# Optimization experiments

Measured on AMD Instinct MI355X. Metric: run time of the kernel, lower is better.

## Reference

```python
import jax, jax.numpy as jnp
import numpy as np

NH = 2  # attention heads


def _mha(q, k, v, w, b, pool):
    """2-head attention; w:[4,D,D] (q,k,v,o as x@W), b:[4,D], pool:[Lq] pools query axis -> [B,D]."""
    B, Lq, D = q.shape
    dk = D // NH
    Q = (q @ w[0] + b[0]).reshape(B, Lq, NH, dk).transpose(0, 2, 1, 3)
    K = (k @ w[1] + b[1]).reshape(B, -1, NH, dk).transpose(0, 2, 1, 3)
    V = (v @ w[2] + b[2]).reshape(B, -1, NH, dk).transpose(0, 2, 1, 3)
    scores = jnp.einsum('bhqd,bhkd->bhqk', Q, K) / jnp.sqrt(jnp.asarray(dk, q.dtype))
    attn = jax.nn.softmax(scores, axis=-1)
    ctx = jnp.einsum('bhqk,bhkd->bqhd', attn, V).reshape(B, Lq, D)
    out = ctx @ w[3] + b[3]              # [B, Lq, D]
    return jnp.einsum('bqd,q->bd', out, pool)  # pooled over query axis (w_size)


def setup_inputs() -> dict:
    key = jax.random.key(0)
    ks = jax.random.split(key, 32)
    B, T, D, N = 64, 32, 768, 901
    s = 0.02
    inp = {
        'question_embeds': jax.random.normal(ks[0], (B, T, D), jnp.float32),
        'image_local_embeds': jax.random.normal(ks[1], (B, N, D), jnp.float32),
        'h0': jax.random.uniform(ks[2], (B, D), jnp.float32),
        'gru_w_ih': jax.random.normal(ks[3], (3 * D, D), jnp.float32) * s,
        'gru_w_hh': jax.random.normal(ks[4], (3 * D, D), jnp.float32) * s,
        'gru_b_ih': jax.random.normal(ks[5], (3 * D,), jnp.float32) * s,
        'gru_b_hh': jax.random.normal(ks[6], (3 * D,), jnp.float32) * s,
        'ga_w': jax.random.normal(ks[7], (4, D, D), jnp.float32) * s,
        'ga_b': jax.random.normal(ks[8], (4, D), jnp.float32) * s,
        'ga_pool': jax.random.normal(ks[9], (1,), jnp.float32),
        'la_w': jax.random.normal(ks[10], (4, D, D), jnp.float32) * s,
        'la_b': jax.random.normal(ks[11], (4, D), jnp.float32) * s,
        'la_pool': jax.random.normal(ks[12], (T,), jnp.float32) * 0.2,
        'go_w': jax.random.normal(ks[13], (4, D, D), jnp.float32) * s,
        'go_b': jax.random.normal(ks[14], (4, D), jnp.float32) * s,
        'go_pool': jax.random.normal(ks[15], (T,), jnp.float32) * 0.2,
        'f1_w': jax.random.normal(ks[16], (2 * D, 1024), jnp.float32) * s,
        'f1_b': jax.random.normal(ks[17], (1024,), jnp.float32) * s,
        'f2_w': jax.random.normal(ks[18], (1024, 512), jnp.float32) * s,
        'f2_b': jax.random.normal(ks[19], (512,), jnp.float32) * s,
        'f3_w': jax.random.normal(ks[20], (512, 1024), jnp.float32) * s,
        'f3_b': jax.random.normal(ks[21], (1024,), jnp.float32) * s,
    }
    return inp


def reference(question_embeds, image_local_embeds, h0,
              gru_w_ih, gru_w_hh, gru_b_ih, gru_b_hh,
              ga_w, ga_b, ga_pool, la_w, la_b, la_pool,
              go_w, go_b, go_pool,
              f1_w, f1_b, f2_w, f2_b, f3_w, f3_b):
    img_cls = image_local_embeds[:, :1, :]        # [B,1,D] global CLS token
    img_loc = image_local_embeds[:, 1:, :]        # [B,N-1,D] patch tokens
    Hs = h0.shape[-1]

    def step(h, x_t):
        # per-timestep cross-attention of question token against image CLS
        a = _mha(x_t[:, None, :], img_cls, img_cls, ga_w, ga_b, ga_pool)  # [B,D]
        wx = a @ gru_w_ih.T                      # [B,3H]
        wh = h @ gru_w_hh.T
        r = jax.nn.sigmoid(wx[:, :Hs] + wh[:, :Hs] + gru_b_ih[:Hs] + gru_b_hh[:Hs])
        z = jax.nn.sigmoid(wx[:, Hs:2 * Hs] + wh[:, Hs:2 * Hs]
                           + gru_b_ih[Hs:2 * Hs] + gru_b_hh[Hs:2 * Hs])
        n = jnp.tanh(wx[:, 2 * Hs:] + gru_b_ih[2 * Hs:]
                     + r * (wh[:, 2 * Hs:] + gru_b_hh[2 * Hs:]))
        h_new = (1 - z) * n + z * h
        return h_new, h_new

    xs = jnp.swapaxes(question_embeds, 0, 1)      # [T,B,D]
    _, ys = jax.lax.scan(step, h0, xs)
    q_emb = jnp.swapaxes(ys, 0, 1)                # [B,T,D]

    local_out = _mha(q_emb, img_loc, img_loc, la_w, la_b, la_pool)   # [B,D]
    gobal_out = _mha(q_emb, img_cls, img_cls, go_w, go_b, go_pool)   # [B,D]
    h = jnp.concatenate([local_out, gobal_out], axis=1)              # [B,2D]
    x = h @ f1_w + f1_b
    x = jax.nn.relu(x @ f2_w + f2_b)
    return x @ f3_w + f3_b                                           # [B,1024]
```

## Files before the change

### kernel.cpp

```cpp
#include <hip/hip_runtime.h>
#include <math.h>


typedef short bf16x8 __attribute__((ext_vector_type(8)));
typedef float f32x4 __attribute__((ext_vector_type(4)));
typedef unsigned short ushort_t;

#define GRU_NB 48

__device__ __forceinline__ unsigned short f2b(float f) {
    unsigned int u = __float_as_uint(f);
    unsigned int r = (u + 0x7FFFu + ((u >> 16) & 1u)) >> 16;
    return (unsigned short)r;
}
__device__ __forceinline__ float b2f(unsigned short s) {
    return __uint_as_float(((unsigned int)s) << 16);
}
__device__ __forceinline__ float sigm(float x) { return 1.f / (1.f + __expf(-x)); }
__device__ __forceinline__ float tanhx(float x) {
    x = fminf(fmaxf(x, -15.f), 15.f);
    float e = __expf(2.f * x);
    return (e - 1.f) / (e + 1.f);
}

__device__ __forceinline__ void gbar(int* flags, int nb, int phase, int bid, int tid) {
    __syncthreads();
    if (tid == 0) __hip_atomic_store(&flags[bid], phase, __ATOMIC_RELAXED, __HIP_MEMORY_SCOPE_AGENT);
    if (tid < 64) {
        for (;;) {
            int v = 0x7fffffff;
            for (int f = tid; f < nb; f += 64)
                v = min(v, __hip_atomic_load(&flags[f], __ATOMIC_RELAXED, __HIP_MEMORY_SCOPE_AGENT));
            if (__all(v >= phase)) break;
            __builtin_amdgcn_s_sleep(1);
        }
    }
    __syncthreads();
}


__global__ void k_cvt_all(const float* __restrict__ whh, const float* __restrict__ la0,
                          const float* __restrict__ la1, const float* __restrict__ h0,
                          const float* __restrict__ gp, const float* __restrict__ lp,
                          ushort_t* __restrict__ whhb, ushort_t* __restrict__ law0b,
                          ushort_t* __restrict__ law1b, ushort_t* __restrict__ h0b,
                          float* __restrict__ hbuf, float* __restrict__ scal,
                          int* __restrict__ bar) {
    if (blockIdx.x == 0) {
        int t = threadIdx.x;
        if (t < 64) {
            float v1 = (t < 32) ? gp[t] : 0.f;
            float v2 = (t < 32) ? lp[t] : 0.f;
#pragma unroll
            for (int m = 1; m < 32; m <<= 1) { v1 += __shfl_xor(v1, m, 64); v2 += __shfl_xor(v2, m, 64); }
            if (t == 0) { scal[0] = v1; scal[1] = v2; }
        }
        for (int i = threadIdx.x; i < 1024; i += 256) bar[i] = 0;
    }
    long i = (long)blockIdx.x * 256 + threadIdx.x;
    const long n1 = 2304L * 768, n2 = n1 + 768L * 768, n3 = n2 + 768L * 768, n4 = n3 + 64L * 768;
    if (i < n1) whhb[i] = f2b(whh[i]);
    else if (i < n2) law0b[i - n1] = f2b(la0[i - n1]);
    else if (i < n3) law1b[i - n2] = f2b(la1[i - n2]);
    else if (i < n4) { float v = h0[i - n3]; h0b[i - n3] = f2b(v); hbuf[i - n3] = v; }
}


template<int MR>
__device__ __forceinline__ void tgemm4(
    const float* __restrict__ A, long lda,
    const float* __restrict__ Bm, int ldb, int transB,
    const float* __restrict__ bias, float s1, float s2,
    const float* __restrict__ bias2, int b2lim,
    float* __restrict__ C, int ldc, int K, int relu, int agent,
    int m0, int n0, float* As, int tid)
{
    for (int r = 0; r < MR; r++)
        for (int k = tid; k < K; k += 256)
            As[r * K + k] = A[(long)(m0 + r) * lda + k];
    __syncthreads();
    int cl = tid & 63, kc = tid >> 6;
    int c = n0 + cl;
    int K4 = K >> 2;
    int kb = kc * K4;
    const float* Bp = transB ? (Bm + (long)c * ldb) : (Bm + c);
    float acc[MR];
#pragma unroll
    for (int r = 0; r < MR; r++) acc[r] = 0.f;
    for (int k = kb; k < kb + K4; k += 8) {
        float bv[8];
        if (!transB) {
#pragma unroll
            for (int i = 0; i < 8; i++) bv[i] = Bp[(long)(k + i) * ldb];
        } else {
            float4 q0 = *(const float4*)(Bp + k);
            float4 q1 = *(const float4*)(Bp + k + 4);
            bv[0] = q0.x; bv[1] = q0.y; bv[2] = q0.z; bv[3] = q0.w;
            bv[4] = q1.x; bv[5] = q1.y; bv[6] = q1.z; bv[7] = q1.w;
        }
#pragma unroll
        for (int i = 0; i < 8; i += 4) {
#pragma unroll
            for (int r = 0; r < MR; r++) {
                float4 x = *(const float4*)&As[r * K + k + i];
                acc[r] += x.x * bv[i] + x.y * bv[i + 1] + x.z * bv[i + 2] + x.w * bv[i + 3];
            }
        }
    }
    __syncthreads();
    float* Red = As;
#pragma unroll
    for (int r = 0; r < MR; r++) Red[(kc * MR + r) * 64 + cl] = acc[r];
    __syncthreads();
    {
        int rg = tid >> 6;
        float bb = (bias ? bias[c] * s2 : 0.f) + ((bias2 && c < b2lim) ? bias2[c] : 0.f);
#pragma unroll
        for (int i = 0; i < MR / 4; i++) {
            int r = rg + i * 4;
            float sum = (Red[(0 * MR + r) * 64 + cl] + Red[(1 * MR + r) * 64 + cl])
                      + (Red[(2 * MR + r) * 64 + cl] + Red[(3 * MR + r) * 64 + cl]);
            float o = sum * s1 + bb;
            if (relu) o = fmaxf(o, 0.f);
            if (agent) __hip_atomic_store(&C[(long)(m0 + r) * ldc + c], o,
                                          __ATOMIC_RELAXED, __HIP_MEMORY_SCOPE_AGENT);
            else C[(long)(m0 + r) * ldc + c] = o;
        }
    }
}


struct HeadP {
    const float *img, *ga_w2, *ga_b2, *go_w2, *go_b2;
    const float *ga_w3, *ga_b3, *go_w3, *go_b3;
    const float *ga_pool, *scal, *w_ih, *b_ih, *b_hh;
    float *t12, *t12g, *avec, *hcat, *base;
    int* flags; int p0, p1;
};

__global__ void __launch_bounds__(256) k_head(HeadP P) {
    __shared__ __align__(16) float As[16 * 768];
    int bid = blockIdx.x, tid = threadIdx.x;
    for (int p = P.p0; p <= P.p1; p++) {
        if (p == 1) {
            if (bid < 192) {
                int prob = bid / 96, r = bid % 96, m8 = r / 12, ct = r % 12;
                tgemm4<8>(P.img, 901L * 768, prob ? P.go_w2 : P.ga_w2, 768, 0,
                          prob ? P.go_b2 : P.ga_b2, 1.f, 1.f, nullptr, 0,
                          prob ? P.t12g : P.t12, 768, 768, 0, 1, m8 * 8, ct * 64, As, tid);
            }
        } else if (p == 2) {
            if (bid < 192) {
                int prob = bid / 96, r = bid % 96, m8 = r / 12, ct = r % 12;
                float sc = prob ? P.scal[0] : P.ga_pool[0];
                tgemm4<8>(prob ? P.t12g : P.t12, 768, prob ? P.go_w3 : P.ga_w3, 768, 0,
                          prob ? P.go_b3 : P.ga_b3, sc, sc, nullptr, 0,
                          prob ? (P.hcat + 768) : P.avec, prob ? 1536 : 768, 768, 0, 1,
                          m8 * 8, ct * 64, As, tid);
            }
        } else if (p == 3) {
            if (bid < 144) {
                int m4 = bid / 36, ct = bid % 36;
                tgemm4<16>(P.avec, 768, P.w_ih, 768, 1, P.b_ih, 1.f, 1.f, P.b_hh, 1536,
                           P.base, 2304, 768, 0, 0, m4 * 16, ct * 64, As, tid);
            }
        }
        if (p < P.p1) gbar(P.flags, 192, p, bid, tid);
    }
}


struct GruP {
    const ushort_t* h0b; const float* h0f; const ushort_t* whh;
    const float* base; const float* bhh; ushort_t* qemb; int* flags;
};

__global__ void __launch_bounds__(384) k_gru_coop(GruP P) {
    __shared__ __align__(16) ushort_t whh_s[3][16][776];
    __shared__ __align__(16) ushort_t as_s[64][200];
    __shared__ float bs[3][64][20];
    __shared__ float h_s[64][20];
    __shared__ float bhh_s[16];
    float* gs = (float*)&as_s[0][0];
    int tid = threadIdx.x;
    int wid = tid >> 6, lane = tid & 63, quad = lane >> 4, l16 = lane & 15;
    int g = wid >> 1, mh = wid & 1;
    int j = blockIdx.x, d0 = j * 16;
    {
        int gS = (wid < 3) ? wid : wid - 3;
        int r0 = (wid < 3) ? 0 : 8;
        for (int r = r0; r < r0 + 8; r++)
            for (int kk = lane * 8; kk < 768; kk += 512)
                *(bf16x8*)&whh_s[gS][r][kk] = *(const bf16x8*)&P.whh[(size_t)(gS * 768 + d0 + r) * 768 + kk];
    }
    for (int e = tid; e < 3072; e += 384) {
        int g2 = e >> 10, rem = e & 1023, b = rem >> 4, c = rem & 15;
        bs[g2][b][c] = P.base[b * 2304 + g2 * 768 + d0 + c];
    }
    for (int e = tid; e < 1024; e += 384) {
        int b = e >> 4, c = e & 15;
        h_s[b][c] = P.h0f[b * 768 + d0 + c];
    }
    if (tid < 16) bhh_s[tid] = P.bhh[1536 + d0 + tid];
    __syncthreads();
    for (int t = 0; t < 32; t++) {
        const ushort_t* Ap = (t == 0) ? P.h0b : (P.qemb + (size_t)(t - 1) * 768);
        size_t ldA = (t == 0) ? 768 : (size_t)32 * 768;
        f32x4 zz4 = {0.f, 0.f, 0.f, 0.f};
        f32x4 acc[2];
        acc[0] = zz4; acc[1] = zz4;
        for (int kq = 0; kq < 4; kq++) {
            __syncthreads();
#pragma unroll
            for (int i = 0; i < 4; i++) {
                int id = i * 384 + tid;
                int row = id / 24, c = id % 24;
                *(bf16x8*)&as_s[row][c * 8] =
                    *(const bf16x8*)(Ap + (size_t)row * ldA + kq * 192 + c * 8);
            }
            __syncthreads();
            for (int kk = 0; kk < 192; kk += 32) {
                bf16x8 bfr = *(const bf16x8*)&whh_s[g][l16][kq * 192 + kk + quad * 8];
#pragma unroll
                for (int mi = 0; mi < 2; mi++) {
                    bf16x8 af = *(const bf16x8*)&as_s[mh * 32 + mi * 16 + l16][kk + quad * 8];
                    acc[mi] = __builtin_amdgcn_mfma_f32_16x16x32_bf16(af, bfr, acc[mi], 0, 0, 0);
                }
            }
        }
        __syncthreads();
#pragma unroll
        for (int mi = 0; mi < 2; mi++)
#pragma unroll
            for (int r = 0; r < 4; r++)
                gs[((size_t)g * 64 + mh * 32 + mi * 16 + quad * 4 + r) * 20 + l16] = acc[mi][r];
        __syncthreads();
        for (int e = tid; e < 512; e += 384) {
            int b = e >> 3, c0 = (e & 7) * 2;
            float hn[2];
#pragma unroll
            for (int u = 0; u < 2; u++) {
                int c = c0 + u;
                float g0 = gs[((size_t)0 * 64 + b) * 20 + c];
                float g1 = gs[((size_t)1 * 64 + b) * 20 + c];
                float g2v = gs[((size_t)2 * 64 + b) * 20 + c];
                float rr = sigm(g0 + bs[0][b][c]);
                float zg = sigm(g1 + bs[1][b][c]);
                float nn = tanhx(bs[2][b][c] + rr * (g2v + bhh_s[c]));
                float hv = h_s[b][c];
                hn[u] = (1.f - zg) * nn + zg * hv;
                h_s[b][c] = hn[u];
            }
            unsigned int pk = (unsigned int)f2b(hn[0]) | ((unsigned int)f2b(hn[1]) << 16);
            __hip_atomic_store((unsigned int*)&P.qemb[((size_t)b * 32 + t) * 768 + d0 + c0],
                               pk, __ATOMIC_RELAXED, __HIP_MEMORY_SCOPE_AGENT);
        }
        __syncthreads();
        if (t < 31) {
            if (tid == 0)
                __hip_atomic_store(&P.flags[j], t + 1, __ATOMIC_RELAXED, __HIP_MEMORY_SCOPE_AGENT);
            if (tid < 64) {
                for (;;) {
                    int v = (tid < GRU_NB)
                        ? __hip_atomic_load(&P.flags[tid], __ATOMIC_RELAXED, __HIP_MEMORY_SCOPE_AGENT)
                        : 0x7fffffff;
                    if (__all(v > t)) break;
                    __builtin_amdgcn_s_sleep(1);
                }
            }
            __syncthreads();
        }
    }
}

__global__ void __launch_bounds__(256) k_gru_step(
    int t, const ushort_t* h0b, const ushort_t* whh, const float* base,
    const float* bhh, float* h, ushort_t* qemb)
{
    int wv = threadIdx.x >> 6, lane = threadIdx.x & 63;
    int quad = lane >> 4, l16 = lane & 15;
    int d0 = blockIdx.x * 64 + wv * 16;
    float bhhn = bhh[1536 + d0 + l16];
    const ushort_t* Ap = (t == 0) ? h0b : (qemb + (long)(t - 1) * 768);
    long ldA = (t == 0) ? 768 : 32 * 768;
    int d = d0 + l16;
    f32x4 zz4 = {0.f, 0.f, 0.f, 0.f};
    f32x4 acc[3][4];
#pragma unroll
    for (int g = 0; g < 3; g++)
#pragma unroll
        for (int mi = 0; mi < 4; mi++) acc[g][mi] = zz4;
    for (int kk = 0; kk < 768; kk += 32) {
        bf16x8 af[4];
#pragma unroll
        for (int mi = 0; mi < 4; mi++)
            af[mi] = *(const bf16x8*)(Ap + (long)(mi * 16 + l16) * ldA + kk + quad * 8);
#pragma unroll
        for (int g = 0; g < 3; g++) {
            bf16x8 bfr = *(const bf16x8*)(whh + (long)(g * 768 + d0 + l16) * 768 + kk + quad * 8);
#pragma unroll
            for (int mi = 0; mi < 4; mi++)
                acc[g][mi] = __builtin_amdgcn_mfma_f32_16x16x32_bf16(af[mi], bfr, acc[g][mi], 0, 0, 0);
        }
    }
#pragma unroll
    for (int mi = 0; mi < 4; mi++) {
#pragma unroll
        for (int r = 0; r < 4; r++) {
            int b = mi * 16 + quad * 4 + r;
            const float* bb = base + b * 2304;
            float rr = sigm(acc[0][mi][r] + bb[d]);
            float zg = sigm(acc[1][mi][r] + bb[768 + d]);
            float nn = tanhx(bb[1536 + d] + rr * (acc[2][mi][r] + bhhn));
            float hv = h[b * 768 + d];
            float hnew = (1.f - zg) * nn + zg * hv;
            h[b * 768 + d] = hnew;
            qemb[(long)(b * 32 + t) * 768 + d] = f2b(hnew);
        }
    }
}


__global__ void __launch_bounds__(256) k_gemm_bf16(
    const ushort_t* __restrict__ A, int lda,
    const ushort_t* __restrict__ B, int ldb, int transB,
    const float* __restrict__ bias,
    ushort_t* __restrict__ Cb, int ldc,
    int K, int remap, int rowoff)
{
    __shared__ __align__(16) ushort_t As[64][72];
    __shared__ __align__(16) ushort_t Bs[64][72];
    int tid = threadIdx.x;
    int wv = tid >> 6, lane = tid & 63, quad = lane >> 4, l16 = lane & 15;
    long bm = (long)blockIdx.y * 64, bn = (long)blockIdx.x * 64;
    f32x4 zz4 = {0.f, 0.f, 0.f, 0.f};
    f32x4 acc[4];
#pragma unroll
    for (int mi = 0; mi < 4; mi++) acc[mi] = zz4;
    int row4 = tid >> 2, seg = tid & 3;
    for (int k0 = 0; k0 < K; k0 += 64) {
        {
            const ushort_t* src = A + (bm + row4) * lda + k0 + seg * 16;
            *(bf16x8*)&As[row4][seg * 16] = *(const bf16x8*)src;
            *(bf16x8*)&As[row4][seg * 16 + 8] = *(const bf16x8*)(src + 8);
        }
        if (transB) {
            const ushort_t* src = B + (bn + row4) * ldb + k0 + seg * 16;
            *(bf16x8*)&Bs[row4][seg * 16] = *(const bf16x8*)src;
            *(bf16x8*)&Bs[row4][seg * 16 + 8] = *(const bf16x8*)(src + 8);
        } else {
            const ushort_t* src = B + (long)(k0 + row4) * ldb + bn + seg * 16;
            bf16x8 v0 = *(const bf16x8*)src;
            bf16x8 v1 = *(const bf16x8*)(src + 8);
#pragma unroll
            for (int i = 0; i < 8; i++) {
                Bs[seg * 16 + i][row4] = (ushort_t)v0[i];
                Bs[seg * 16 + 8 + i][row4] = (ushort_t)v1[i];
            }
        }
        __syncthreads();
#pragma unroll
        for (int ks = 0; ks < 64; ks += 32) {
            bf16x8 bfr = *(const bf16x8*)&Bs[wv * 16 + l16][ks + quad * 8];
#pragma unroll
            for (int mi = 0; mi < 4; mi++) {
                bf16x8 af = *(const bf16x8*)&As[mi * 16 + l16][ks + quad * 8];
                acc[mi] = __builtin_amdgcn_mfma_f32_16x16x32_bf16(af, bfr, acc[mi], 0, 0, 0);
            }
        }
        __syncthreads();
    }
    int ncol = (int)bn + wv * 16 + l16;
    float bv = bias ? bias[ncol] : 0.f;
#pragma unroll
    for (int mi = 0; mi < 4; mi++) {
#pragma unroll
        for (int r = 0; r < 4; r++) {
            long row = bm + mi * 16 + quad * 4 + r;
            long orow = remap ? ((row >> 5) * 64 + rowoff + (row & 31)) : row;
            Cb[orow * ldc + ncol] = f2b(acc[mi][r] + bv);
        }
    }
}


__global__ void __launch_bounds__(512) k_flash(
    const float* __restrict__ img, const ushort_t* __restrict__ Qt,
    const ushort_t* __restrict__ Qb, const float* __restrict__ la_b1,
    float* __restrict__ pm, float* __restrict__ pl,
    ushort_t* __restrict__ pacc, int nsplit)
{
    __shared__ __align__(16) ushort_t xs[32][776];
    __shared__ float Sls[64][36];
    __shared__ __align__(16) ushort_t Pls[64][40];
    __shared__ float m_s[64], l_s[64], al_s[64], qb_s[64];
    int b = blockIdx.x;
    int sp = blockIdx.y;
    int tper = (29 + nsplit - 1) / nsplit;
    int tb = sp * tper, te = min(29, tb + tper);
    int tid = threadIdx.x;
    int wv = tid >> 6, lane = tid & 63, quad = lane >> 4, l16 = lane & 15;
    {
        int row = tid >> 3, sub = tid & 7;
        int hh = row >> 5, q = row & 31;
        const ushort_t* src = Qb + ((size_t)(b * 32 + q)) * 768 + hh * 384 + sub * 48;
        const float* bb = la_b1 + hh * 384 + sub * 48;
        float s = 0.f;
#pragma unroll
        for (int k = 0; k < 48; k++) s += b2f(src[k]) * bb[k];
        s += __shfl_xor(s, 1, 64); s += __shfl_xor(s, 2, 64); s += __shfl_xor(s, 4, 64);
        if (sub == 0) qb_s[row] = s;
    }
    if (tid < 64) { m_s[tid] = -1e30f; l_s[tid] = 0.f; }
    f32x4 zz4 = {0.f, 0.f, 0.f, 0.f};
    f32x4 acc[4][6];
#pragma unroll
    for (int mi = 0; mi < 4; mi++)
#pragma unroll
        for (int nj = 0; nj < 6; nj++) acc[mi][nj] = zz4;
    const float rs = 0.051031036307982884f;
    int smi = wv & 3, sni = wv >> 2;
    __syncthreads();
    for (int t0 = tb; t0 < te; t0++) {
        int key0 = t0 * 32;
        {
            int keyl = tid >> 4, dseg = tid & 15;
            int key = key0 + keyl;
            const float* src = img + ((long)b * 901 + 1 + key) * 768;
            bool ok = key < 900;
#pragma unroll
            for (int c = 0; c < 12; c++) {
                int dd = c * 64 + dseg * 4;
                float x0 = 0, x1 = 0, x2 = 0, x3 = 0;
                if (ok) { float4 v = *(const float4*)(src + dd); x0 = v.x; x1 = v.y; x2 = v.z; x3 = v.w; }
                ushort_t* dst = &xs[keyl][dd];
                dst[0] = f2b(x0); dst[1] = f2b(x1); dst[2] = f2b(x2); dst[3] = f2b(x3);
            }
        }
        __syncthreads();
        {
            f32x4 as = zz4;
            const ushort_t* qrow = Qt + (long)(b * 64 + smi * 16 + l16) * 768 + quad * 8;
            const ushort_t* xrow = &xs[sni * 16 + l16][quad * 8];
#pragma unroll
            for (int kk = 0; kk < 768; kk += 32) {
                bf16x8 aq = *(const bf16x8*)(qrow + kk);
                bf16x8 bx = *(const bf16x8*)(xrow + kk);
                as = __builtin_amdgcn_mfma_f32_16x16x32_bf16(aq, bx, as, 0, 0, 0);
            }
#pragma unroll
            for (int r = 0; r < 4; r++) {
                int row = smi * 16 + quad * 4 + r;
                Sls[row][sni * 16 + l16] = (as[r] + qb_s[row]) * rs;
            }
        }
        __syncthreads();
        {
            int row = tid >> 3, sub = tid & 7;
            float sv[4];
            float mx = -1e30f;
#pragma unroll
            for (int i = 0; i < 4; i++) {
                int kl = sub + i * 8;
                float s = (key0 + kl < 900) ? Sls[row][kl] : -1e30f;
                sv[i] = s; mx = fmaxf(mx, s);
            }
            mx = fmaxf(mx, __shfl_xor(mx, 1, 64));
            mx = fmaxf(mx, __shfl_xor(mx, 2, 64));
            mx = fmaxf(mx, __shfl_xor(mx, 4, 64));
            float mold = m_s[row];
            float mnew = fmaxf(mold, mx);
            float ss = 0.f;
#pragma unroll
            for (int i = 0; i < 4; i++) {
                float p = __expf(sv[i] - mnew);
                ss += p;
                Pls[row][sub + i * 8] = f2b(p);
            }
            ss += __shfl_xor(ss, 1, 64);
            ss += __shfl_xor(ss, 2, 64);
            ss += __shfl_xor(ss, 4, 64);
            if (sub == 0) {
                float alpha = __expf(mold - mnew);
                al_s[row] = alpha;
                l_s[row] = l_s[row] * alpha + ss;
                m_s[row] = mnew;
            }
        }
        __syncthreads();
        {
            bf16x8 pf[4];
#pragma unroll
            for (int mi = 0; mi < 4; mi++)
                pf[mi] = *(const bf16x8*)&Pls[mi * 16 + l16][quad * 8];
#pragma unroll
            for (int mi = 0; mi < 4; mi++) {
#pragma unroll
                for (int r = 0; r < 4; r++) {
                    float a = al_s[mi * 16 + quad * 4 + r];
#pragma unroll
                    for (int nj = 0; nj < 6; nj++) acc[mi][nj][r] *= a;
                }
            }
#pragma unroll
            for (int nj = 0; nj < 6; nj++) {
                int dd = wv * 96 + nj * 16 + l16;
                bf16x8 bx;
#pragma unroll
                for (int j = 0; j < 8; j++) bx[j] = (short)xs[quad * 8 + j][dd];
#pragma unroll
                for (int mi = 0; mi < 4; mi++)
                    acc[mi][nj] = __builtin_amdgcn_mfma_f32_16x16x32_bf16(pf[mi], bx, acc[mi][nj], 0, 0, 0);
            }
        }
        __syncthreads();
    }
    if (tid < 64) {
        pm[(b * nsplit + sp) * 64 + tid] = m_s[tid];
        pl[(b * nsplit + sp) * 64 + tid] = l_s[tid];
    }
#pragma unroll
    for (int mi = 0; mi < 4; mi++) {
#pragma unroll
        for (int r = 0; r < 4; r++) {
            int row = mi * 16 + quad * 4 + r;
            ushort_t* dst = pacc + ((size_t)(b * nsplit + sp) * 64 + row) * 768;
#pragma unroll
            for (int nj = 0; nj < 6; nj++)
                dst[wv * 96 + nj * 16 + l16] = f2b(acc[mi][nj][r]);
        }
    }
}


struct TailP {
    const float *pm, *pl; const ushort_t* pacc; const float* lp;
    const float *la_w2, *la_b2, *la_w3, *la_b3, *scal;
    float *plX, *pc, *hcat;
    const float *f1w, *f1b, *f2w, *f2b, *f3w, *f3b;
    float *x1, *x2, *out;
    int* flags; int p0, p1, nsplit;
};

template<int NS>
__global__ void __launch_bounds__(256) k_tail(TailP P) {
    __shared__ __align__(16) float As[4 * 1536];
    __shared__ float cw[NS][64];
    int bid = blockIdx.x, tid = threadIdx.x;
    float sla = P.scal[1];
    for (int p = P.p0; p <= P.p1; p++) {
        if (p == 0) {
            if (bid < 192) {
                int b = bid / 3, jj = bid % 3;
                if (tid < 64) {
                    int row = tid;
                    float ex[NS];
                    float mmax = -1e30f;
#pragma unroll
                    for (int s = 0; s < NS; s++) mmax = fmaxf(mmax, P.pm[(b * NS + s) * 64 + row]);
                    float lsum = 0.f;
#pragma unroll
                    for (int s = 0; s < NS; s++) {
                        ex[s] = __expf(P.pm[(b * NS + s) * 64 + row] - mmax);
                        lsum += ex[s] * P.pl[(b * NS + s) * 64 + row];
                    }
                    float sc = P.lp[row & 31] / lsum;
#pragma unroll
                    for (int s = 0; s < NS; s++) cw[s][row] = ex[s] * sc;
                }
                __syncthreads();
                int col = jj * 256 + tid;
                const ushort_t* pp = P.pacc + ((size_t)(b * NS)) * 64 * 768 + col;
                float ac0 = 0.f, ac1 = 0.f;
                for (int q = 0; q < 32; q += 2) {
                    float vv[2][NS][2];
#pragma unroll
                    for (int u = 0; u < 2; u++)
#pragma unroll
                        for (int s = 0; s < NS; s++) {
                            vv[u][s][0] = b2f(pp[((size_t)(s * 64 + q + u)) * 768]);
                            vv[u][s][1] = b2f(pp[((size_t)(s * 64 + 32 + q + u)) * 768]);
                        }
#pragma unroll
                    for (int u = 0; u < 2; u++)
#pragma unroll
                        for (int s = 0; s < NS; s++) {
                            ac0 += cw[s][q + u] * vv[u][s][0];
                            ac1 += cw[s][32 + q + u] * vv[u][s][1];
                        }
                }
                __hip_atomic_store(&P.plX[b * 1536 + col], ac0,
                                   __ATOMIC_RELAXED, __HIP_MEMORY_SCOPE_AGENT);
                __hip_atomic_store(&P.plX[b * 1536 + 768 + col], ac1,
                                   __ATOMIC_RELAXED, __HIP_MEMORY_SCOPE_AGENT);
            }
        } else if (p == 1) {
            if (bid < 192) {
                int m4 = bid / 12, ct = bid % 12, prob = ct / 6;
                tgemm4<4>(P.plX + prob * 768, 1536, P.la_w2, 768, 0,
                          P.la_b2, 1.f, sla, nullptr, 0,
                          P.pc, 768, 768, 0, 1, m4 * 4, ct * 64, As, tid);
            }
        } else if (p == 2) {
            if (bid < 192) {
                int m4 = bid / 12, ct = bid % 12;
                tgemm4<4>(P.pc, 768, P.la_w3, 768, 0, P.la_b3, 1.f, sla, nullptr, 0,
                          P.hcat, 1536, 768, 0, 1, m4 * 4, ct * 64, As, tid);
            }
        } else if (p == 3) {
            if (bid < 256) {
                int m4 = bid / 16, ct = bid % 16;
                tgemm4<4>(P.hcat, 1536, P.f1w, 1024, 0, P.f1b, 1.f, 1.f, nullptr, 0,
                          P.x1, 1024, 1536, 0, 1, m4 * 4, ct * 64, As, tid);
            }
        } else if (p == 4) {
            if (bid < 128) {
                int m4 = bid / 8, ct = bid % 8;
                tgemm4<4>(P.x1, 1024, P.f2w, 512, 0, P.f2b, 1.f, 1.f, nullptr, 0,
                          P.x2, 512, 1024, 1, 1, m4 * 4, ct * 64, As, tid);
            }
        } else if (p == 5) {
            if (bid < 256) {
                int m4 = bid / 16, ct = bid % 16;
                tgemm4<4>(P.x2, 512, P.f3w, 1024, 0, P.f3b, 1.f, 1.f, nullptr, 0,
                          P.out, 1024, 512, 0, 0, m4 * 4, ct * 64, As, tid);
            }
        }
        if (p < P.p1) gbar(P.flags, 256, p + 1, bid, tid);
    }
}


extern "C" void kernel_launch(void* const* d_in, const int* in_sizes, int n_in,
                              void* d_out, int out_size, void* d_ws, size_t ws_size,
                              hipStream_t stream)
{
    const float* img  = (const float*)d_in[1];
    const float* h0   = (const float*)d_in[2];
    const float* w_ih = (const float*)d_in[3];
    const float* w_hh = (const float*)d_in[4];
    const float* b_ih = (const float*)d_in[5];
    const float* b_hh = (const float*)d_in[6];
    const float* ga_w = (const float*)d_in[7];
    const float* ga_b = (const float*)d_in[8];
    const float* ga_pool = (const float*)d_in[9];
    const float* la_w = (const float*)d_in[10];
    const float* la_b = (const float*)d_in[11];
    const float* la_pool = (const float*)d_in[12];
    const float* go_w = (const float*)d_in[13];
    const float* go_b = (const float*)d_in[14];
    const float* go_pool = (const float*)d_in[15];
    const float* f1w = (const float*)d_in[16];
    const float* f1b = (const float*)d_in[17];
    const float* f2w = (const float*)d_in[18];
    const float* f2b_ = (const float*)d_in[19];
    const float* f3w = (const float*)d_in[20];
    const float* f3b = (const float*)d_in[21];
    float* out = (float*)d_out;
    (void)in_sizes; (void)n_in; (void)out_size;

    int nsplit = (ws_size >= (size_t)43 * 1024 * 1024) ? 4 : 2;

    char* w = (char*)d_ws;
    auto alloc = [&](size_t bytes) -> char* {
        char* p = w; w += (bytes + 255) & ~(size_t)255; return p;
    };
    float*    scal  = (float*)alloc(256);
    int*      bar   = (int*)alloc(4096);
    ushort_t* law0b = (ushort_t*)alloc((size_t)768 * 768 * 2);
    ushort_t* law1b = (ushort_t*)alloc((size_t)768 * 768 * 2);
    ushort_t* h0b   = (ushort_t*)alloc((size_t)64 * 768 * 2);
    ushort_t* qembb = (ushort_t*)alloc((size_t)2048 * 768 * 2);
    ushort_t* Qb    = (ushort_t*)alloc((size_t)2048 * 768 * 2);
    ushort_t* Qtb   = (ushort_t*)alloc((size_t)4096 * 768 * 2);
    float*    pm    = (float*)alloc((size_t)64 * 4 * 64 * 4);
    float*    pl    = (float*)alloc((size_t)64 * 4 * 64 * 4);
    float*    plX   = (float*)alloc((size_t)64 * 1536 * 4);
    float*    pc    = (float*)alloc((size_t)64 * 768 * 4);
    float*    hcat  = (float*)alloc((size_t)64 * 1536 * 4);
    float*    x1    = (float*)alloc((size_t)64 * 1024 * 4);
    float*    x2    = (float*)alloc((size_t)64 * 512 * 4);
    char* uni = w;
    char* u = uni;
    auto ualloc = [&](size_t bytes) -> char* {
        char* p = u; u += (bytes + 255) & ~(size_t)255; return p;
    };
    ushort_t* whhb  = (ushort_t*)ualloc((size_t)2304 * 768 * 2);
    float*    t12   = (float*)ualloc((size_t)2 * 64 * 768 * 4);
    float*    avec  = (float*)ualloc((size_t)64 * 768 * 4);
    float*    base  = (float*)ualloc((size_t)64 * 2304 * 4);
    float*    hbuf  = (float*)ualloc((size_t)64 * 768 * 4);
    ushort_t* pacc  = (ushort_t*)uni;
    float*    t12g  = t12 + 64 * 768;

    const float* ga_w2 = ga_w + 2 * 768 * 768; const float* ga_w3 = ga_w + 3 * 768 * 768;
    const float* ga_b2 = ga_b + 2 * 768;       const float* ga_b3 = ga_b + 3 * 768;
    const float* go_w2 = go_w + 2 * 768 * 768; const float* go_w3 = go_w + 3 * 768 * 768;
    const float* go_b2 = go_b + 2 * 768;       const float* go_b3 = go_b + 3 * 768;
    const float* la_w0 = la_w;                 const float* la_w1 = la_w + 768 * 768;
    const float* la_w2 = la_w + 2 * 768 * 768; const float* la_w3 = la_w + 3 * 768 * 768;
    const float* la_b0 = la_b;                 const float* la_b1 = la_b + 768;
    const float* la_b2 = la_b + 2 * 768;       const float* la_b3 = la_b + 3 * 768;

    dim3 blk(256);
    k_cvt_all<<<11712, blk, 0, stream>>>(w_hh, la_w0, la_w1, h0, go_pool, la_pool,
                                         whhb, law0b, law1b, h0b, hbuf, scal, bar);

    {
        HeadP P;
        P.img = img; P.ga_w2 = ga_w2; P.ga_b2 = ga_b2; P.go_w2 = go_w2; P.go_b2 = go_b2;
        P.ga_w3 = ga_w3; P.ga_b3 = ga_b3; P.go_w3 = go_w3; P.go_b3 = go_b3;
        P.ga_pool = ga_pool; P.scal = scal; P.w_ih = w_ih; P.b_ih = b_ih; P.b_hh = b_hh;
        P.t12 = t12; P.t12g = t12g; P.avec = avec; P.hcat = hcat; P.base = base;
        P.flags = bar + 64; P.p0 = 1; P.p1 = 3;
        void* args[1] = { &P };
        hipError_t e = hipLaunchCooperativeKernel((void*)k_head, dim3(192), blk, args, 0, stream);
        if (e != hipSuccess)
            for (int p = 1; p <= 3; p++) { P.p0 = P.p1 = p; k_head<<<192, blk, 0, stream>>>(P); }
    }

    {
        GruP P;
        P.h0b = h0b; P.h0f = h0; P.whh = whhb; P.base = base; P.bhh = b_hh;
        P.qemb = qembb; P.flags = bar;
        void* args[1] = { &P };
        hipError_t e = hipLaunchCooperativeKernel((void*)k_gru_coop, dim3(GRU_NB), dim3(384),
                                                  args, 0, stream);
        if (e != hipSuccess)
            for (int t = 0; t < 32; t++)
                k_gru_step<<<12, blk, 0, stream>>>(t, h0b, whhb, base, b_hh, hbuf, qembb);
    }

    k_gemm_bf16<<<dim3(12, 32), blk, 0, stream>>>(qembb, 768, law0b, 768, 0, la_b0, Qb, 768, 768, 0, 0);
    k_gemm_bf16<<<dim3(12, 32), blk, 0, stream>>>(Qb, 768, law1b, 768, 1, nullptr, Qtb, 768, 384, 1, 0);
    k_gemm_bf16<<<dim3(12, 32), blk, 0, stream>>>(Qb + 384, 768, law1b + 384, 768, 1, nullptr, Qtb, 768, 384, 1, 32);

    k_flash<<<dim3(64, nsplit), dim3(512), 0, stream>>>(img, Qtb, Qb, la_b1, pm, pl, pacc, nsplit);

    {
        TailP P;
        P.pm = pm; P.pl = pl; P.pacc = pacc; P.lp = la_pool;
        P.la_w2 = la_w2; P.la_b2 = la_b2; P.la_w3 = la_w3; P.la_b3 = la_b3; P.scal = scal;
        P.plX = plX; P.pc = pc; P.hcat = hcat;
        P.f1w = f1w; P.f1b = f1b; P.f2w = f2w; P.f2b = f2b_; P.f3w = f3w; P.f3b = f3b;
        P.x1 = x1; P.x2 = x2; P.out = out;
        P.flags = bar + 320; P.p0 = 0; P.p1 = 5; P.nsplit = nsplit;
        void* args[1] = { &P };
        if (nsplit == 4) {
            hipError_t e = hipLaunchCooperativeKernel((void*)k_tail<4>, dim3(256), blk, args, 0, stream);
            if (e != hipSuccess)
                for (int p = 0; p <= 5; p++) { P.p0 = P.p1 = p; k_tail<4><<<256, blk, 0, stream>>>(P); }
        } else {
            hipError_t e = hipLaunchCooperativeKernel((void*)k_tail<2>, dim3(256), blk, args, 0, stream);
            if (e != hipSuccess)
                for (int p = 0; p <= 5; p++) { P.p0 = P.p1 = p; k_tail<2><<<256, blk, 0, stream>>>(P); }
        }
    }
}
```

Before: 1.006 ms.

## Double tail kernel grid to 512 blocks with 2-row GEMM tiles

```diff
diff --git a/kernel.cpp b/kernel.cpp
--- a/kernel.cpp
+++ b/kernel.cpp
@@ -112,20 +112,16 @@
 #pragma unroll
     for (int r = 0; r < MR; r++) Red[(kc * MR + r) * 64 + cl] = acc[r];
     __syncthreads();
-    {
-        int rg = tid >> 6;
-        float bb = (bias ? bias[c] * s2 : 0.f) + ((bias2 && c < b2lim) ? bias2[c] : 0.f);
-#pragma unroll
-        for (int i = 0; i < MR / 4; i++) {
-            int r = rg + i * 4;
-            float sum = (Red[(0 * MR + r) * 64 + cl] + Red[(1 * MR + r) * 64 + cl])
-                      + (Red[(2 * MR + r) * 64 + cl] + Red[(3 * MR + r) * 64 + cl]);
-            float o = sum * s1 + bb;
-            if (relu) o = fmaxf(o, 0.f);
-            if (agent) __hip_atomic_store(&C[(long)(m0 + r) * ldc + c], o,
-                                          __ATOMIC_RELAXED, __HIP_MEMORY_SCOPE_AGENT);
-            else C[(long)(m0 + r) * ldc + c] = o;
-        }
+    for (int o = tid; o < MR * 64; o += 256) {
+        int r = o >> 6, c2 = o & 63, cc = n0 + c2;
+        float sum = (Red[(0 * MR + r) * 64 + c2] + Red[(1 * MR + r) * 64 + c2])
+                  + (Red[(2 * MR + r) * 64 + c2] + Red[(3 * MR + r) * 64 + c2]);
+        float bb = (bias ? bias[cc] * s2 : 0.f) + ((bias2 && cc < b2lim) ? bias2[cc] : 0.f);
+        float ov = sum * s1 + bb;
+        if (relu) ov = fmaxf(ov, 0.f);
+        if (agent) __hip_atomic_store(&C[(long)(m0 + r) * ldc + cc], ov,
+                                      __ATOMIC_RELAXED, __HIP_MEMORY_SCOPE_AGENT);
+        else C[(long)(m0 + r) * ldc + cc] = ov;
     }
 }
 
@@ -543,17 +539,17 @@
 };
 
 template<int NS>
-__global__ void __launch_bounds__(256) k_tail(TailP P) {
-    __shared__ __align__(16) float As[4 * 1536];
-    __shared__ float cw[NS][64];
+__global__ void __launch_bounds__(256, 4) k_tail(TailP P) {
+    __shared__ __align__(16) float As[2 * 1536];
+    __shared__ float cw[NS][32];
     int bid = blockIdx.x, tid = threadIdx.x;
     float sla = P.scal[1];
     for (int p = P.p0; p <= P.p1; p++) {
         if (p == 0) {
-            if (bid < 192) {
-                int b = bid / 3, jj = bid % 3;
-                if (tid < 64) {
-                    int row = tid;
+            if (bid < 384) {
+                int b = bid / 6, r6 = bid % 6, jj = r6 % 3, half = r6 / 3;
+                if (tid < 32) {
+                    int row = half * 32 + tid;
                     float ex[NS];
                     float mmax = -1e30f;
 #pragma unroll
@@ -564,69 +560,65 @@
                         ex[s] = __expf(P.pm[(b * NS + s) * 64 + row] - mmax);
                         lsum += ex[s] * P.pl[(b * NS + s) * 64 + row];
                     }
-                    float sc = P.lp[row & 31] / lsum;
-#pragma unroll
-                    for (int s = 0; s < NS; s++) cw[s][row] = ex[s] * sc;
+                    float sc = P.lp[tid] / lsum;
+#pragma unroll
+                    for (int s = 0; s < NS; s++) cw[s][tid] = ex[s] * sc;
                 }
                 __syncthreads();
                 int col = jj * 256 + tid;
-                const ushort_t* pp = P.pacc + ((size_t)(b * NS)) * 64 * 768 + col;
-                float ac0 = 0.f, ac1 = 0.f;
+                const ushort_t* pp = P.pacc + ((size_t)(b * NS)) * 64 * 768
+                                   + (size_t)half * 32 * 768 + col;
+                float ac = 0.f;
                 for (int q = 0; q < 32; q += 2) {
-                    float vv[2][NS][2];
+                    float vv[2][NS];
 #pragma unroll
                     for (int u = 0; u < 2; u++)
 #pragma unroll
-                        for (int s = 0; s < NS; s++) {
-                            vv[u][s][0] = b2f(pp[((size_t)(s * 64 + q + u)) * 768]);
-                            vv[u][s][1] = b2f(pp[((size_t)(s * 64 + 32 + q + u)) * 768]);
-                        }
+                        for (int s = 0; s < NS; s++)
+                            vv[u][s] = b2f(pp[((size_t)(s * 64 + q + u)) * 768]);
 #pragma unroll
                     for (int u = 0; u < 2; u++)
 #pragma unroll
-                        for (int s = 0; s < NS; s++) {
-                            ac0 += cw[s][q + u] * vv[u][s][0];
-                            ac1 += cw[s][32 + q + u] * vv[u][s][1];
-                        }
+                        for (int s = 0; s < NS; s++)
+                            ac += cw[s][q + u] * vv[u][s];
                 }
-                __hip_atomic_store(&P.plX[b * 1536 + col], ac0,
+                __hip_atomic_store(&P.plX[b * 1536 + half * 768 + col], ac,
                                    __ATOMIC_RELAXED, __HIP_MEMORY_SCOPE_AGENT);
-                __hip_atomic_store(&P.plX[b * 1536 + 768 + col], ac1,
-                                   __ATOMIC_RELAXED, __HIP_MEMORY_SCOPE_AGENT);
+                __syncthreads();
             }
         } else if (p == 1) {
-            if (bid < 192) {
-                int m4 = bid / 12, ct = bid % 12, prob = ct / 6;
-                tgemm4<4>(P.plX + prob * 768, 1536, P.la_w2, 768, 0,
+            if (bid < 384) {
+                int m2 = bid / 12, ct = bid % 12, prob = ct / 6;
+                tgemm4<2>(P.plX + prob * 768, 1536, P.la_w2, 768, 0,
                           P.la_b2, 1.f, sla, nullptr, 0,
-                          P.pc, 768, 768, 0, 1, m4 * 4, ct * 64, As, tid);
+                          P.pc, 768, 768, 0, 1, m2 * 2, ct * 64, As, tid);
             }
         } else if (p == 2) {
-            if (bid < 192) {
-                int m4 = bid / 12, ct = bid % 12;
-                tgemm4<4>(P.pc, 768, P.la_w3, 768, 0, P.la_b3, 1.f, sla, nullptr, 0,
-                          P.hcat, 1536, 768, 0, 1, m4 * 4, ct * 64, As, tid);
+            if (bid < 384) {
+                int m2 = bid / 12, ct = bid % 12;
+                tgemm4<2>(P.pc, 768, P.la_w3, 768, 0, P.la_b3, 1.f, sla, nullptr, 0,
+                          P.hcat, 1536, 768, 0, 1, m2 * 2, ct * 64, As, tid);
             }
         } else if (p == 3) {
+            if (bid < 512) {
+                int m2 = bid / 16, ct = bid % 16;
+                tgemm4<2>(P.hcat, 1536, P.f1w, 1024, 0, P.f1b, 1.f, 1.f, nullptr, 0,
+                          P.x1, 1024, 1536, 0, 1, m2 * 2, ct * 64, As, tid);
+            }
+        } else if (p == 4) {
             if (bid < 256) {
-                int m4 = bid / 16, ct = bid % 16;
-                tgemm4<4>(P.hcat, 1536, P.f1w, 1024, 0, P.f1b, 1.f, 1.f, nullptr, 0,
-                          P.x1, 1024, 1536, 0, 1, m4 * 4, ct * 64, As, tid);
-            }
-        } else if (p == 4) {
-            if (bid < 128) {
-                int m4 = bid / 8, ct = bid % 8;
-                tgemm4<4>(P.x1, 1024, P.f2w, 512, 0, P.f2b, 1.f, 1.f, nullptr, 0,
-                          P.x2, 512, 1024, 1, 1, m4 * 4, ct * 64, As, tid);
+                int m2 = bid / 8, ct = bid % 8;
+                tgemm4<2>(P.x1, 1024, P.f2w, 512, 0, P.f2b, 1.f, 1.f, nullptr, 0,
+                          P.x2, 512, 1024, 1, 1, m2 * 2, ct * 64, As, tid);
             }
         } else if (p == 5) {
-            if (bid < 256) {
-                int m4 = bid / 16, ct = bid % 16;
-                tgemm4<4>(P.x2, 512, P.f3w, 1024, 0, P.f3b, 1.f, 1.f, nullptr, 0,
-                          P.out, 1024, 512, 0, 0, m4 * 4, ct * 64, As, tid);
-            }
-        }
-        if (p < P.p1) gbar(P.flags, 256, p + 1, bid, tid);
+            if (bid < 512) {
+                int m2 = bid / 16, ct = bid % 16;
+                tgemm4<2>(P.x2, 512, P.f3w, 1024, 0, P.f3b, 1.f, 1.f, nullptr, 0,
+                          P.out, 1024, 512, 0, 0, m2 * 2, ct * 64, As, tid);
+            }
+        }
+        if (p < P.p1) gbar(P.flags, 512, p + 1, bid, tid);
     }
 }
 
@@ -747,13 +739,13 @@
         P.flags = bar + 320; P.p0 = 0; P.p1 = 5; P.nsplit = nsplit;
         void* args[1] = { &P };
         if (nsplit == 4) {
-            hipError_t e = hipLaunchCooperativeKernel((void*)k_tail<4>, dim3(256), blk, args, 0, stream);
+            hipError_t e = hipLaunchCooperativeKernel((void*)k_tail<4>, dim3(512), blk, args, 0, stream);
             if (e != hipSuccess)
-                for (int p = 0; p <= 5; p++) { P.p0 = P.p1 = p; k_tail<4><<<256, blk, 0, stream>>>(P); }
+                for (int p = 0; p <= 5; p++) { P.p0 = P.p1 = p; k_tail<4><<<512, blk, 0, stream>>>(P); }
         } else {
-            hipError_t e = hipLaunchCooperativeKernel((void*)k_tail<2>, dim3(256), blk, args, 0, stream);
+            hipError_t e = hipLaunchCooperativeKernel((void*)k_tail<2>, dim3(512), blk, args, 0, stream);
             if (e != hipSuccess)
-                for (int p = 0; p <= 5; p++) { P.p0 = P.p1 = p; k_tail<2><<<256, blk, 0, stream>>>(P); }
-        }
-    }
-}
+                for (int p = 0; p <= 5; p++) { P.p0 = P.p1 = p; k_tail<2><<<512, blk, 0, stream>>>(P); }
+        }
+    }
+}
```

Measured after the change: 1.107 ms. +10.1%, slower.
